# Kernel optimization log

Hardware: AMD Instinct MI355X
Metric: run time of the kernel (lower is better)

Reference implementation:

```python
import jax, jax.numpy as jnp
import numpy as np

B, C, T, F = 8, 64, 512, 128
CH = C // 2            # 32, per-branch channels
HID = 64               # hidden_channels
GH = 2 * CH            # GRU hidden size = 64
KT, KF = 3, 3
PAD_T = (KT - 1) * 1   # causal pad on time
EPS_LN = 1e-6
EPS_BN = 1e-5


def _ln2d(x, g, b):
    # LayerNorm over channel dim of (B,C,T,F) (== permute->LN(C)->permute)
    mu = jnp.mean(x, axis=1, keepdims=True)
    var = jnp.var(x, axis=1, keepdims=True)
    xn = (x - mu) / jnp.sqrt(var + EPS_LN)
    return xn * g[None, :, None, None] + b[None, :, None, None]


def _prelu(x, a):
    return jnp.where(x >= 0, x, a * x)


def setup_inputs() -> dict:
    key = jax.random.key(0)
    ks = jax.random.split(key, 8)
    s = 0.1
    return {
        "x": jax.random.normal(ks[0], (B, C, T, F), jnp.float32),
        "pw1_w": jax.random.normal(ks[1], (HID, CH * 3), jnp.float32) * s,
        "pw1_b": jnp.zeros((HID,), jnp.float32),
        "ln1_g": jnp.ones((HID,), jnp.float32),
        "ln1_b": jnp.zeros((HID,), jnp.float32),
        "prelu1": jnp.full((1,), 0.25, jnp.float32),
        "dw_w": jax.random.normal(ks[2], (HID, 1, KT, KF), jnp.float32) * s,
        "dw_b": jnp.zeros((HID,), jnp.float32),
        "bn_g": jnp.ones((HID,), jnp.float32),
        "bn_b": jnp.zeros((HID,), jnp.float32),
        "bn_mean": jnp.zeros((HID,), jnp.float32),
        "bn_var": jnp.ones((HID,), jnp.float32),
        "prelu2": jnp.full((1,), 0.25, jnp.float32),
        "pw2_w": jax.random.normal(ks[3], (CH, HID), jnp.float32) * s,
        "pw2_b": jnp.zeros((CH,), jnp.float32),
        "ln2_g": jnp.ones((CH,), jnp.float32),
        "ln2_b": jnp.zeros((CH,), jnp.float32),
        "gru_wih": jax.random.normal(ks[4], (3 * GH, CH), jnp.float32) * s,
        "gru_whh": jax.random.normal(ks[5], (3 * GH, GH), jnp.float32) * s,
        "gru_bih": jnp.zeros((3 * GH,), jnp.float32),
        "gru_bhh": jnp.zeros((3 * GH,), jnp.float32),
        "fc_w": jax.random.normal(ks[6], (CH, GH), jnp.float32) * s,
        "fc_b": jnp.zeros((CH,), jnp.float32),
    }


def reference(x, pw1_w, pw1_b, ln1_g, ln1_b, prelu1, dw_w, dw_b,
              bn_g, bn_b, bn_mean, bn_var, prelu2, pw2_w, pw2_b,
              ln2_g, ln2_b, gru_wih, gru_whh, gru_bih, gru_bhh, fc_w, fc_b):
    x1, x2 = x[:, :CH], x[:, CH:]
    # SFE: unfold along F with kernel 3 (pad 1) -> (B, 3*CH, T, F), order (c, k)
    xp = jnp.pad(x1, ((0, 0), (0, 0), (0, 0), (1, 1)))
    xs = jnp.stack([xp[..., k:k + F] for k in range(3)], axis=2)  # (B,CH,3,T,F)
    xs = xs.reshape(B, 3 * CH, T, F)
    # pointwise conv1 + LayerNorm2d + PReLU
    h = jnp.einsum('bctf,oc->botf', xs, pw1_w) + pw1_b[None, :, None, None]
    h = _prelu(_ln2d(h, ln1_g, ln1_b), prelu1)
    # causal pad on T, depthwise (3,3) conv with F padding 1
    h = jnp.pad(h, ((0, 0), (0, 0), (PAD_T, 0), (0, 0)))
    h = jax.lax.conv_general_dilated(
        h, dw_w, window_strides=(1, 1), padding=((0, 0), (1, 1)),
        dimension_numbers=('NCHW', 'OIHW', 'NCHW'), feature_group_count=HID)
    h = h + dw_b[None, :, None, None]
    # BatchNorm2d (inference form) + PReLU
    inv = bn_g / jnp.sqrt(bn_var + EPS_BN)
    h = (h - bn_mean[None, :, None, None]) * inv[None, :, None, None] + bn_b[None, :, None, None]
    h = _prelu(h, prelu2)
    # pointwise conv2 + LayerNorm2d
    h = jnp.einsum('bctf,oc->botf', h, pw2_w) + pw2_b[None, :, None, None]
    h = _ln2d(h, ln2_g, ln2_b)
    # TRA: GRU attention over time
    zt = jnp.mean(h * h, axis=-1)            # (B,CH,T)
    xseq = zt.transpose(0, 2, 1)             # (B,T,CH)
    xg = jnp.einsum('btc,gc->btg', xseq, gru_wih) + gru_bih  # (B,T,3GH)

    def step(hprev, xg_t):
        hg = hprev @ gru_whh.T + gru_bhh
        r = jax.nn.sigmoid(xg_t[:, :GH] + hg[:, :GH])
        z = jax.nn.sigmoid(xg_t[:, GH:2 * GH] + hg[:, GH:2 * GH])
        n = jnp.tanh(xg_t[:, 2 * GH:] + r * hg[:, 2 * GH:])
        hnew = (1.0 - z) * n + z * hprev
        return hnew, hnew

    h0 = jnp.zeros((B, GH), jnp.float32)
    _, hs = jax.lax.scan(step, h0, xg.transpose(1, 0, 2))  # (T,B,GH)
    at = jnp.einsum('tbg,og->bto', hs, fc_w) + fc_b        # (B,T,CH)
    at = jax.nn.sigmoid(at).transpose(0, 2, 1)             # (B,CH,T)
    h = h * at[..., None]
    # channel shuffle: interleave h and x2 -> (B, C, T, F)
    out = jnp.stack([h, x2], axis=2).reshape(B, C, T, F)
    return out
```

## Files before the change

### kernel.cpp

```cpp
#include <hip/hip_runtime.h>
#include <hip/hip_bf16.h>

typedef short bf16x8 __attribute__((ext_vector_type(8)));
typedef float f32x4 __attribute__((ext_vector_type(4)));
typedef _Float16 h2f __attribute__((ext_vector_type(2)));

#define DEVINL static __device__ __forceinline__

DEVINL float bf2f(ushort u) {
    union { unsigned int i; float f; } v;
    v.i = ((unsigned int)u) << 16;
    return v.f;
}
DEVINL ushort f2bf(float f) {
    union { float f; unsigned int i; } v;
    v.f = f;
    unsigned int r = v.i + 0x7FFFu + ((v.i >> 16) & 1u);
    return (ushort)(r >> 16);
}
DEVINL float sigmoid_f(float x) {
    x = fminf(fmaxf(x, -30.f), 30.f);
    return 1.f / (1.f + __expf(-x));
}
DEVINL float tanh_f(float x) {
    x = fminf(fmaxf(x, -15.f), 15.f);
    float e = __expf(-2.f * x);
    return (1.f - e) / (1.f + e);
}
DEVINL h2f as_h2(unsigned int u) {
    union { unsigned int u; h2f h; } v;
    v.u = u;
    return v.h;
}
DEVINL float hdot(h2f a, h2f b, float c) {
#if __has_builtin(__builtin_amdgcn_fdot2)
    return __builtin_amdgcn_fdot2(a, b, c, false);
#else
    h2f p = a * b;
    return c + (float)p[0] + (float)p[1];
#endif
}

#define TT 16

__global__ __launch_bounds__(512, 2) void stageA_kernel(
    const float* __restrict__ x, const float* __restrict__ pw1w,
    const float* __restrict__ pw1b, const float* __restrict__ ln1g,
    const float* __restrict__ ln1b, const float* __restrict__ pr1,
    const float* __restrict__ dww, const float* __restrict__ dwb_,
    const float* __restrict__ bng, const float* __restrict__ bnb,
    const float* __restrict__ bnm, const float* __restrict__ bnv,
    const float* __restrict__ pr2, const float* __restrict__ pw2w,
    const float* __restrict__ pw2b, const float* __restrict__ ln2g,
    const float* __restrict__ ln2b,
    float* __restrict__ outp, float* __restrict__ ztout)
{
    __shared__ __align__(16) ushort x1T[130][40];
    __shared__ __align__(16) ushort ring[3][64][132];
    __shared__ __align__(16) ushort HdT[128][72];
    __shared__ float ztp[8][32];

    const int tid = threadIdx.x;
    const int lane = tid & 63;
    const int wv = tid >> 6;
    const int lg = lane >> 4;
    const int lr = lane & 15;
    const int b = blockIdx.x >> 5;
    const int t0 = (blockIdx.x & 31) * TT;
    const int fcol = 16 * wv + lr;

    bf16x8 a1f[4][3];
    #pragma unroll
    for (int ot = 0; ot < 4; ++ot)
        #pragma unroll
        for (int kk = 0; kk < 3; ++kk)
            #pragma unroll
            for (int j = 0; j < 8; ++j)
                a1f[ot][kk][j] = (short)f2bf(pw1w[(16 * ot + lr) * 96 + 3 * (8 * lg + j) + kk]);

    float b1v[16], g1v[16], be1v[16];
    #pragma unroll
    for (int ot = 0; ot < 4; ++ot)
        #pragma unroll
        for (int jj = 0; jj < 4; ++jj) {
            int o = 16 * ot + 4 * lg + jj;
            b1v[ot * 4 + jj] = pw1b[o];
            g1v[ot * 4 + jj] = ln1g[o];
            be1v[ot * 4 + jj] = ln1b[o];
        }
    const float alpha1 = pr1[0];
    const float alpha2 = pr2[0];

    float wd[9];
    #pragma unroll
    for (int i = 0; i < 9; ++i) wd[i] = dww[lane * 9 + i];
    const float dwbias = dwb_[lane];
    const float bninv = bng[lane] * rsqrtf(bnv[lane] + 1e-5f);
    const float bnsh = bnb[lane] - bnm[lane] * bninv;

    bf16x8 a2f[2][2];
    #pragma unroll
    for (int ot = 0; ot < 2; ++ot)
        #pragma unroll
        for (int ks = 0; ks < 2; ++ks)
            #pragma unroll
            for (int j = 0; j < 8; ++j)
                a2f[ot][ks][j] = (short)f2bf(pw2w[(16 * ot + lr) * 64 + 32 * ks + 8 * lg + j]);

    float b2v[8], g2v[8], be2v[8];
    #pragma unroll
    for (int ot = 0; ot < 2; ++ot)
        #pragma unroll
        for (int jj = 0; jj < 4; ++jj) {
            int o = 16 * ot + 4 * lg + jj;
            b2v[ot * 4 + jj] = pw2b[o];
            g2v[ot * 4 + jj] = ln2g[o];
            be2v[ot * 4 + jj] = ln2b[o];
        }

    for (int i = tid; i < 3 * 64; i += 512) {
        int sl = i >> 6, o = i & 63;
        ring[sl][o][0] = 0; ring[sl][o][1] = 0;
        ring[sl][o][130] = 0; ring[sl][o][131] = 0;
    }

    for (int s = 0; s < TT + 2; ++s) {
        const int tt = t0 - 2 + s;
        __syncthreads();
        if (tt >= 0) {
            const int ch = tid >> 4, f0 = (tid & 15) << 3;
            const float* xp = x + (((size_t)(b * 64 + ch) * 512 + tt) * 128 + f0);
            float4 v0 = *(const float4*)xp;
            float4 v1 = *(const float4*)(xp + 4);
            x1T[f0 + 1][ch] = f2bf(v0.x); x1T[f0 + 2][ch] = f2bf(v0.y);
            x1T[f0 + 3][ch] = f2bf(v0.z); x1T[f0 + 4][ch] = f2bf(v0.w);
            x1T[f0 + 5][ch] = f2bf(v1.x); x1T[f0 + 6][ch] = f2bf(v1.y);
            x1T[f0 + 7][ch] = f2bf(v1.z); x1T[f0 + 8][ch] = f2bf(v1.w);
            if (tid < 40) { x1T[0][tid] = 0; x1T[129][tid] = 0; }
        }
        __syncthreads();
        const int slot = s % 3;
        if (tt >= 0) {
            f32x4 acc[4] = {};
            #pragma unroll
            for (int kk = 0; kk < 3; ++kk) {
                bf16x8 bfr = *(const bf16x8*)&x1T[16 * wv + lr + kk][8 * lg];
                #pragma unroll
                for (int ot = 0; ot < 4; ++ot)
                    acc[ot] = __builtin_amdgcn_mfma_f32_16x16x32_bf16(a1f[ot][kk], bfr, acc[ot], 0, 0, 0);
            }
            float vals[16];
            float sm = 0.f, sq = 0.f;
            #pragma unroll
            for (int ot = 0; ot < 4; ++ot)
                #pragma unroll
                for (int jj = 0; jj < 4; ++jj) {
                    float v2 = acc[ot][jj] + b1v[ot * 4 + jj];
                    vals[ot * 4 + jj] = v2; sm += v2; sq += v2 * v2;
                }
            sm += __shfl_xor(sm, 16); sm += __shfl_xor(sm, 32);
            sq += __shfl_xor(sq, 16); sq += __shfl_xor(sq, 32);
            const float mu = sm * (1.f / 64.f);
            const float rs = rsqrtf(sq * (1.f / 64.f) - mu * mu + 1e-6f);
            #pragma unroll
            for (int ot = 0; ot < 4; ++ot)
                #pragma unroll
                for (int jj = 0; jj < 4; ++jj) {
                    float y = (vals[ot * 4 + jj] - mu) * rs * g1v[ot * 4 + jj] + be1v[ot * 4 + jj];
                    y = (y >= 0.f) ? y : alpha1 * y;
                    ring[slot][16 * ot + 4 * lg + jj][2 + fcol] = f2bf(y);
                }
        } else {
            for (int i = tid; i < 64 * 132; i += 512)
                ((ushort*)ring[slot])[i] = 0;
        }
        if (s >= 2) {
            const int tau = tt;
            __syncthreads();
            float hd[16] = {};
            #pragma unroll
            for (int kt = 0; kt < 3; ++kt) {
                const int slk = (s - 2 + kt) % 3;
                float rowv[20];
                #pragma unroll
                for (int i = 0; i < 5; ++i) {
                    uint2 q = *(const uint2*)&ring[slk][lane][16 * wv + 4 * i];
                    const ushort* p = (const ushort*)&q;
                    rowv[4 * i + 0] = bf2f(p[0]); rowv[4 * i + 1] = bf2f(p[1]);
                    rowv[4 * i + 2] = bf2f(p[2]); rowv[4 * i + 3] = bf2f(p[3]);
                }
                #pragma unroll
                for (int fo = 0; fo < 16; ++fo)
                    hd[fo] += wd[kt * 3 + 0] * rowv[fo + 1] + wd[kt * 3 + 1] * rowv[fo + 2]
                            + wd[kt * 3 + 2] * rowv[fo + 3];
            }
            #pragma unroll
            for (int fo = 0; fo < 16; ++fo) {
                float v2 = hd[fo] + dwbias;
                v2 = v2 * bninv + bnsh;
                v2 = (v2 >= 0.f) ? v2 : alpha2 * v2;
                HdT[16 * wv + fo][lane] = f2bf(v2);
            }
            __syncthreads();
            f32x4 acc2[2] = {};
            #pragma unroll
            for (int ks = 0; ks < 2; ++ks) {
                bf16x8 bfr = *(const bf16x8*)&HdT[16 * wv + lr][32 * ks + 8 * lg];
                #pragma unroll
                for (int ot = 0; ot < 2; ++ot)
                    acc2[ot] = __builtin_amdgcn_mfma_f32_16x16x32_bf16(a2f[ot][ks], bfr, acc2[ot], 0, 0, 0);
            }
            float vals2[8];
            float sm2 = 0.f, sq2 = 0.f;
            #pragma unroll
            for (int ot = 0; ot < 2; ++ot)
                #pragma unroll
                for (int jj = 0; jj < 4; ++jj) {
                    float v2 = acc2[ot][jj] + b2v[ot * 4 + jj];
                    vals2[ot * 4 + jj] = v2; sm2 += v2; sq2 += v2 * v2;
                }
            sm2 += __shfl_xor(sm2, 16); sm2 += __shfl_xor(sm2, 32);
            sq2 += __shfl_xor(sq2, 16); sq2 += __shfl_xor(sq2, 32);
            const float mu2 = sm2 * (1.f / 32.f);
            const float rs2 = rsqrtf(sq2 * (1.f / 32.f) - mu2 * mu2 + 1e-6f);
            float zpart[8];
            #pragma unroll
            for (int ot = 0; ot < 2; ++ot)
                #pragma unroll
                for (int jj = 0; jj < 4; ++jj) {
                    float y = (vals2[ot * 4 + jj] - mu2) * rs2 * g2v[ot * 4 + jj] + be2v[ot * 4 + jj];
                    const int o = 16 * ot + 4 * lg + jj;
                    outp[(((size_t)(b * 64 + 2 * o) * 512 + tau) * 128) + fcol] = y;
                    zpart[ot * 4 + jj] = y * y;
                }
            #pragma unroll
            for (int k = 0; k < 8; ++k) {
                float v2 = zpart[k];
                v2 += __shfl_xor(v2, 1); v2 += __shfl_xor(v2, 2);
                v2 += __shfl_xor(v2, 4); v2 += __shfl_xor(v2, 8);
                zpart[k] = v2;
            }
            if (lr == 0) {
                #pragma unroll
                for (int ot = 0; ot < 2; ++ot)
                    #pragma unroll
                    for (int jj = 0; jj < 4; ++jj)
                        ztp[wv][16 * ot + 4 * lg + jj] = zpart[ot * 4 + jj];
            }
            __syncthreads();
            if (tid < 32) {
                float a = 0.f;
                #pragma unroll
                for (int w = 0; w < 8; ++w) a += ztp[w][tid];
                ztout[((size_t)b * 512 + tau) * 32 + tid] = a * (1.f / 128.f);
            }
        }
    }
}

__global__ __launch_bounds__(256) void xg_kernel(
    const float* __restrict__ zt, const float* __restrict__ wih,
    const float* __restrict__ bih, float* __restrict__ xg)
{
    const int idx = blockIdx.x * 256 + threadIdx.x;
    const int g = idx % 192;
    const int bt = idx / 192;
    if (bt >= 4096) return;
    const float* z = zt + (size_t)bt * 32;
    float acc = bih[g];
    #pragma unroll 8
    for (int c = 0; c < 32; ++c) acc += wih[g * 32 + c] * z[c];
    xg[(size_t)bt * 192 + g] = acc;
}

__global__ __launch_bounds__(64) void gru_kernel(
    const float* __restrict__ xg, const float* __restrict__ whh,
    const float* __restrict__ bhh, float* __restrict__ hs)
{
    const int b = blockIdx.x;
    const int c = threadIdx.x;
    __shared__ __align__(16) _Float16 hbuf[2][64];
    h2f w0[32], w1[32], w2[32];
    #pragma unroll
    for (int i = 0; i < 32; ++i) {
        w0[i][0] = (_Float16)whh[c * 64 + 2 * i];
        w0[i][1] = (_Float16)whh[c * 64 + 2 * i + 1];
        w1[i][0] = (_Float16)whh[(64 + c) * 64 + 2 * i];
        w1[i][1] = (_Float16)whh[(64 + c) * 64 + 2 * i + 1];
        w2[i][0] = (_Float16)whh[(128 + c) * 64 + 2 * i];
        w2[i][1] = (_Float16)whh[(128 + c) * 64 + 2 * i + 1];
    }
    const float bh0 = bhh[c];
    const float bh1 = bhh[64 + c];
    const float bh2 = bhh[128 + c];
    h2f hv[32];
    #pragma unroll
    for (int i = 0; i < 32; ++i) { hv[i][0] = (_Float16)0.f; hv[i][1] = (_Float16)0.f; }
    float hmy = 0.f;
    const float* xgb = xg + (size_t)b * 512 * 192;
    float* hsb = hs + (size_t)b * 512 * 64;
    float xr = xgb[c], xz = xgb[64 + c], xn = xgb[128 + c];
    for (int t = 0; t < 512; ++t) {
        float nxr = 0.f, nxz = 0.f, nxn = 0.f;
        if (t < 511) {
            const float* p = xgb + (size_t)(t + 1) * 192;
            nxr = p[c]; nxz = p[64 + c]; nxn = p[128 + c];
        }
        float a0 = bh0, a1 = 0.f, a2 = bh1, a3 = 0.f, a4 = bh2, a5 = 0.f;
        #pragma unroll
        for (int i = 0; i < 32; i += 2) {
            a0 = hdot(w0[i], hv[i], a0); a1 = hdot(w0[i + 1], hv[i + 1], a1);
            a2 = hdot(w1[i], hv[i], a2); a3 = hdot(w1[i + 1], hv[i + 1], a3);
            a4 = hdot(w2[i], hv[i], a4); a5 = hdot(w2[i + 1], hv[i + 1], a5);
        }
        const float r = sigmoid_f(xr + a0 + a1);
        const float z = sigmoid_f(xz + a2 + a3);
        const float n = tanh_f(xn + r * (a4 + a5));
        const float hn = (1.f - z) * n + z * hmy;
        hmy = hn;
        hsb[(size_t)t * 64 + c] = hn;
        const int bi = t & 1;
        hbuf[bi][c] = (_Float16)hn;
        __syncthreads();
        const uint4* q4 = (const uint4*)hbuf[bi];
        #pragma unroll
        for (int i = 0; i < 8; ++i) {
            uint4 q = q4[i];
            hv[4 * i + 0] = as_h2(q.x); hv[4 * i + 1] = as_h2(q.y);
            hv[4 * i + 2] = as_h2(q.z); hv[4 * i + 3] = as_h2(q.w);
        }
        xr = nxr; xz = nxz; xn = nxn;
    }
}

__global__ __launch_bounds__(256) void stageC_kernel(
    const float* __restrict__ hs, const float* __restrict__ fcw,
    const float* __restrict__ fcb, const float* __restrict__ x,
    float* __restrict__ outp)
{
    __shared__ float fw[32][66];
    __shared__ float hsl[8][64];
    __shared__ float atl[8][32];
    const int tid = threadIdx.x;
    const int b = blockIdx.x >> 6;
    const int t0 = (blockIdx.x & 63) * 8;
    for (int i = tid; i < 2048; i += 256) fw[i >> 6][i & 63] = fcw[i];
    for (int i = tid; i < 512; i += 256) hsl[i >> 6][i & 63] = hs[((size_t)b * 512 + t0) * 64 + i];
    __syncthreads();
    {
        const int t = tid >> 5, o = tid & 31;
        float acc = fcb[o];
        #pragma unroll 8
        for (int g = 0; g < 64; ++g) acc += fw[o][g] * hsl[t][g];
        atl[t][o] = sigmoid_f(acc);
    }
    __syncthreads();
    #pragma unroll
    for (int k = 0; k < 32; ++k) {
        const int i = tid + (k << 8);
        const int f0 = (i & 15) << 3;
        const int c = (i >> 4) & 63;
        const int tl = i >> 10;
        const int t = t0 + tl;
        const int ch = c >> 1;
        float* op = outp + ((size_t)(b * 64 + c) * 512 + t) * 128 + f0;
        if (c & 1) {
            const float* xp = x + (((size_t)(b * 64 + 32 + ch) * 512 + t) * 128 + f0);
            float4 v0 = *(const float4*)xp;
            float4 v1 = *(const float4*)(xp + 4);
            *(float4*)op = v0;
            *(float4*)(op + 4) = v1;
        } else {
            const float a = atl[tl][ch];
            float4 v0 = *(const float4*)op;
            float4 v1 = *(const float4*)(op + 4);
            v0.x *= a; v0.y *= a; v0.z *= a; v0.w *= a;
            v1.x *= a; v1.y *= a; v1.z *= a; v1.w *= a;
            *(float4*)op = v0;
            *(float4*)(op + 4) = v1;
        }
    }
}

extern "C" void kernel_launch(void* const* d_in, const int* in_sizes, int n_in,
                              void* d_out, int out_size, void* d_ws, size_t ws_size,
                              hipStream_t stream) {
    (void)in_sizes; (void)n_in; (void)out_size; (void)ws_size;
    const float* x    = (const float*)d_in[0];
    const float* pw1w = (const float*)d_in[1];
    const float* pw1b = (const float*)d_in[2];
    const float* ln1g = (const float*)d_in[3];
    const float* ln1b = (const float*)d_in[4];
    const float* pr1  = (const float*)d_in[5];
    const float* dww  = (const float*)d_in[6];
    const float* dwb  = (const float*)d_in[7];
    const float* bng  = (const float*)d_in[8];
    const float* bnb  = (const float*)d_in[9];
    const float* bnm  = (const float*)d_in[10];
    const float* bnv  = (const float*)d_in[11];
    const float* pr2  = (const float*)d_in[12];
    const float* pw2w = (const float*)d_in[13];
    const float* pw2b = (const float*)d_in[14];
    const float* ln2g = (const float*)d_in[15];
    const float* ln2b = (const float*)d_in[16];
    const float* wih  = (const float*)d_in[17];
    const float* whh  = (const float*)d_in[18];
    const float* bih  = (const float*)d_in[19];
    const float* bhh  = (const float*)d_in[20];
    const float* fcw  = (const float*)d_in[21];
    const float* fcb  = (const float*)d_in[22];
    float* outp = (float*)d_out;
    char* ws = (char*)d_ws;
    float* ztbuf = (float*)ws;
    float* xgbuf = (float*)(ws + 524288);
    float* hsbuf = (float*)(ws + 524288 + 3145728);

    stageA_kernel<<<256, 512, 0, stream>>>(x, pw1w, pw1b, ln1g, ln1b, pr1, dww, dwb,
                                           bng, bnb, bnm, bnv, pr2, pw2w, pw2b, ln2g, ln2b,
                                           outp, ztbuf);
    xg_kernel<<<3072, 256, 0, stream>>>(ztbuf, wih, bih, xgbuf);
    gru_kernel<<<8, 64, 0, stream>>>(xgbuf, whh, bhh, hsbuf);
    stageC_kernel<<<512, 256, 0, stream>>>(hsbuf, fcw, fcb, x, outp);
}
```

Before: 652.7 us.

## Broadcast GRU hidden state via readlane instead of LDS and barrier

```diff
diff --git a/kernel.cpp b/kernel.cpp
--- a/kernel.cpp
+++ b/kernel.cpp
@@ -279,7 +279,6 @@
 {
     const int b = blockIdx.x;
     const int c = threadIdx.x;
-    __shared__ __align__(16) _Float16 hbuf[2][64];
     h2f w0[32], w1[32], w2[32];
     #pragma unroll
     for (int i = 0; i < 32; ++i) {
@@ -293,43 +292,47 @@
     const float bh0 = bhh[c];
     const float bh1 = bhh[64 + c];
     const float bh2 = bhh[128 + c];
-    h2f hv[32];
-    #pragma unroll
-    for (int i = 0; i < 32; ++i) { hv[i][0] = (_Float16)0.f; hv[i][1] = (_Float16)0.f; }
+    unsigned int hvu[32];
+    #pragma unroll
+    for (int i = 0; i < 32; ++i) hvu[i] = 0u;
     float hmy = 0.f;
     const float* xgb = xg + (size_t)b * 512 * 192;
     float* hsb = hs + (size_t)b * 512 * 64;
-    float xr = xgb[c], xz = xgb[64 + c], xn = xgb[128 + c];
+    float xr0 = xgb[c], xz0 = xgb[64 + c], xn0 = xgb[128 + c];
+    float xr1 = xgb[192 + c], xz1 = xgb[192 + 64 + c], xn1 = xgb[192 + 128 + c];
     for (int t = 0; t < 512; ++t) {
         float nxr = 0.f, nxz = 0.f, nxn = 0.f;
-        if (t < 511) {
-            const float* p = xgb + (size_t)(t + 1) * 192;
+        if (t < 510) {
+            const float* p = xgb + (size_t)(t + 2) * 192;
             nxr = p[c]; nxz = p[64 + c]; nxn = p[128 + c];
         }
         float a0 = bh0, a1 = 0.f, a2 = bh1, a3 = 0.f, a4 = bh2, a5 = 0.f;
         #pragma unroll
         for (int i = 0; i < 32; i += 2) {
-            a0 = hdot(w0[i], hv[i], a0); a1 = hdot(w0[i + 1], hv[i + 1], a1);
-            a2 = hdot(w1[i], hv[i], a2); a3 = hdot(w1[i + 1], hv[i + 1], a3);
-            a4 = hdot(w2[i], hv[i], a4); a5 = hdot(w2[i + 1], hv[i + 1], a5);
-        }
-        const float r = sigmoid_f(xr + a0 + a1);
-        const float z = sigmoid_f(xz + a2 + a3);
-        const float n = tanh_f(xn + r * (a4 + a5));
+            const h2f h0 = as_h2(hvu[i]), h1 = as_h2(hvu[i + 1]);
+            a0 = hdot(w0[i], h0, a0); a1 = hdot(w0[i + 1], h1, a1);
+            a2 = hdot(w1[i], h0, a2); a3 = hdot(w1[i + 1], h1, a3);
+            a4 = hdot(w2[i], h0, a4); a5 = hdot(w2[i + 1], h1, a5);
+        }
+        const float r = sigmoid_f(xr0 + a0 + a1);
+        const float z = sigmoid_f(xz0 + a2 + a3);
+        const float n = tanh_f(xn0 + r * (a4 + a5));
         const float hn = (1.f - z) * n + z * hmy;
         hmy = hn;
         hsb[(size_t)t * 64 + c] = hn;
-        const int bi = t & 1;
-        hbuf[bi][c] = (_Float16)hn;
-        __syncthreads();
-        const uint4* q4 = (const uint4*)hbuf[bi];
-        #pragma unroll
-        for (int i = 0; i < 8; ++i) {
-            uint4 q = q4[i];
-            hv[4 * i + 0] = as_h2(q.x); hv[4 * i + 1] = as_h2(q.y);
-            hv[4 * i + 2] = as_h2(q.z); hv[4 * i + 3] = as_h2(q.w);
-        }
-        xr = nxr; xz = nxz; xn = nxn;
+        const float ph = __shfl_xor(hn, 1);
+        const float lo = (c & 1) ? ph : hn;
+        const float hi = (c & 1) ? hn : ph;
+        h2f pk;
+        pk[0] = (_Float16)lo;
+        pk[1] = (_Float16)hi;
+        int pku;
+        __builtin_memcpy(&pku, &pk, 4);
+        #pragma unroll
+        for (int i = 0; i < 32; ++i)
+            hvu[i] = (unsigned int)__builtin_amdgcn_readlane(pku, 2 * i);
+        xr0 = xr1; xz0 = xz1; xn0 = xn1;
+        xr1 = nxr; xz1 = nxz; xn1 = nxn;
     }
 }
 
```

New measurement: 718.0 us. +10.0%, slower.
